# Optimization experiments

Measured on AMD Instinct MI355X. Metric: run time of the kernel, lower is better.

## Reference

```python
import jax, jax.numpy as jnp
import numpy as np

EPS = 1e-5

def _instance_norm(t):
    # torch .var(dim=2) default is unbiased (ddof=1) over flattened HW
    b, c, h, w = t.shape
    flat = t.reshape(b, c, h * w)
    mean = flat.mean(axis=2)
    var = flat.var(axis=2, ddof=1) + EPS
    return (t - mean[:, :, None, None]) / jnp.sqrt(var)[:, :, None, None]

def _conv1x1(t, w, b):
    # w: [Cout, Cin], b: [Cout]; t: [B, Cin, H, W]
    return jnp.einsum('oc,bchw->bohw', w, t) + b[None, :, None, None]


def setup_inputs() -> dict:
    key = jax.random.key(0)
    ks = jax.random.split(key, 11)
    B, C, H, W = 4, 512, 64, 64
    scale = 1.0 / np.sqrt(C)
    inp = {
        'c': jax.random.normal(ks[0], (B, C, H, W), jnp.float32),
        's': jax.random.normal(ks[1], (B, C, H, W), jnp.float32),
        'x': jax.random.normal(ks[2], (B, C, H, W), jnp.float32),
        'c_w': jax.random.normal(ks[3], (C, C), jnp.float32) * scale,
        'c_b': jax.random.normal(ks[4], (C,), jnp.float32) * 0.01,
        's_w': jax.random.normal(ks[5], (C, C), jnp.float32) * scale,
        's_b': jax.random.normal(ks[6], (C,), jnp.float32) * 0.01,
        'i_w': jax.random.normal(ks[7], (C, C), jnp.float32) * scale,
        'i_b': jax.random.normal(ks[8], (C,), jnp.float32) * 0.01,
        'o_w': jax.random.normal(ks[9], (C, C), jnp.float32) * scale,
        'o_b': jax.random.normal(ks[10], (C,), jnp.float32) * 0.01,
    }
    return inp


def reference(c, s, x, c_w, c_b, s_w, s_b, i_w, i_b, o_w, o_b):
    B, C, H, W = c.shape
    N = H * W
    cf = _conv1x1(_instance_norm(c), c_w, c_b).reshape(B, C, N)
    sf = _conv1x1(_instance_norm(s), s_w, s_b).reshape(B, C, N)
    xf = _conv1x1(s, i_w, i_b).reshape(B, C, N)
    # mask[b, n, m] = sum_c cf[b, c, n] * sf[b, c, m]; softmax over m
    mask = jax.nn.softmax(jnp.einsum('bcn,bcm->bnm', cf, sf), axis=-1)
    # of = xf @ mask^T : of[b, c, n] = sum_m xf[b, c, m] * mask[b, n, m]
    of = jnp.einsum('bcm,bnm->bcn', xf, mask).reshape(B, C, H, W)
    of = _conv1x1(of, o_w, o_b)
    return x + of
```

## Files before the change

kernel.cpp:

```cpp
#include <hip/hip_runtime.h>

typedef unsigned short u16;
typedef _Float16 f16x8 __attribute__((ext_vector_type(8)));
typedef float f32x4 __attribute__((ext_vector_type(4)));
typedef u16 u16x4 __attribute__((ext_vector_type(4)));
typedef u16 u16x8v __attribute__((ext_vector_type(8)));

__device__ __forceinline__ u16 f2h(float f) {
    _Float16 h = (_Float16)f;
    return __builtin_bit_cast(u16, h);
}
__device__ __forceinline__ float h2f(u16 u) {
    return (float)__builtin_bit_cast(_Float16, u);
}

__global__ void __launch_bounds__(256) stats_kernel(
    const float* __restrict__ c, const float* __restrict__ s,
    float* __restrict__ mC, float* __restrict__ rC,
    float* __restrict__ mS, float* __restrict__ rS)
{
    const float* src = (blockIdx.y ? s : c) + (size_t)blockIdx.x * 4096;
    int t = threadIdx.x, lane = t & 63, wv = t >> 6;
    const float4* p = (const float4*)src;
    float sum = 0.f, sq = 0.f;
#pragma unroll
    for (int i = 0; i < 4; ++i) {
        float4 v = p[t + 256 * i];
        sum += v.x + v.y + v.z + v.w;
        sq  += v.x * v.x + v.y * v.y + v.z * v.z + v.w * v.w;
    }
#pragma unroll
    for (int m = 1; m < 64; m <<= 1) {
        sum += __shfl_xor(sum, m);
        sq  += __shfl_xor(sq, m);
    }
    __shared__ float sa[4], sb[4];
    if (!lane) { sa[wv] = sum; sb[wv] = sq; }
    __syncthreads();
    if (t == 0) {
        float S = sa[0] + sa[1] + sa[2] + sa[3];
        float Q = sb[0] + sb[1] + sb[2] + sb[3];
        float mean = S * (1.0f / 4096.0f);
        float var = (Q - 4096.0f * mean * mean) * (1.0f / 4095.0f);
        float rstd = rsqrtf(var + 1e-5f);
        if (blockIdx.y) { mS[blockIdx.x] = mean; rS[blockIdx.x] = rstd; }
        else            { mC[blockIdx.x] = mean; rC[blockIdx.x] = rstd; }
    }
}

__global__ void __launch_bounds__(256) packall(
    const float* __restrict__ c, const float* __restrict__ s,
    const float* __restrict__ mC, const float* __restrict__ rC,
    const float* __restrict__ mS, const float* __restrict__ rS,
    u16* __restrict__ cnT, u16* __restrict__ snT, u16* __restrict__ sRT)
{
    __shared__ float tile[32][33];
    int z = blockIdx.z;
    bool isS = z >= 4;
    int b = isS ? z - 4 : z;
    const float* src  = isS ? s : c;
    const float* mean = isS ? mS : mC;
    const float* rstd = isS ? rS : rC;
    u16* dh = isS ? snT : cnT;
    int n0 = blockIdx.x * 32, c0 = blockIdx.y * 32;
    int tx = threadIdx.x, ty = threadIdx.y;
    const float* sbp = src + ((size_t)b * 512 + c0) * 4096 + n0;
#pragma unroll
    for (int it = 0; it < 4; ++it) {
        int cc = ty + it * 8;
        tile[cc][tx] = sbp[(size_t)cc * 4096 + tx];
    }
    __syncthreads();
    int ch = c0 + tx;
    float mn = mean[b * 512 + ch];
    float rs = rstd[b * 512 + ch];
    size_t obase = ((size_t)b * 4096 + n0) * 512 + c0;
#pragma unroll
    for (int it = 0; it < 4; ++it) {
        int r = ty + it * 8;
        float v = tile[tx][r];
        size_t o = obase + (size_t)r * 512 + tx;
        dh[o] = f2h((v - mn) * rs);
        if (isS) sRT[o] = f2h(v);
    }
}

__global__ void __launch_bounds__(256) prep_kernel(
    const float* __restrict__ c_w, const float* __restrict__ s_w,
    const float* __restrict__ i_w, const float* __restrict__ o_w,
    u16* __restrict__ cwT, u16* __restrict__ swT,
    u16* __restrict__ iwT, u16* __restrict__ ow)
{
    int z = blockIdx.z;
    int tx = threadIdx.x, ty = threadIdx.y;
    if (z == 3) {
        size_t base = ((size_t)(blockIdx.y * 16 + blockIdx.x) * 256 +
                       (ty * 32 + tx)) * 4;
        float4 v = *(const float4*)(o_w + base);
        u16x4 o;
        o[0] = f2h(v.x); o[1] = f2h(v.y); o[2] = f2h(v.z); o[3] = f2h(v.w);
        *(u16x4*)(ow + base) = o;
        return;
    }
    const float* w = (z == 0) ? c_w : (z == 1) ? s_w : i_w;
    u16* wT = (z == 0) ? cwT : (z == 1) ? swT : iwT;
    __shared__ float tile[32][33];
    int c0 = blockIdx.x * 32, k0 = blockIdx.y * 32;
#pragma unroll
    for (int it = 0; it < 4; ++it) {
        int kk = ty + it * 8;
        tile[kk][tx] = w[(size_t)(k0 + kk) * 512 + c0 + tx];
    }
    __syncthreads();
#pragma unroll
    for (int it = 0; it < 4; ++it) {
        int r = ty + it * 8;
        wT[(size_t)(c0 + r) * 512 + k0 + tx] = f2h(tile[tx][r]);
    }
}

__global__ void __launch_bounds__(256) bias_prep(
    const float* __restrict__ o_w, const float* __restrict__ i_b,
    const float* __restrict__ o_b, const float* __restrict__ s_w,
    const float* __restrict__ c_b, float* __restrict__ v,
    float* __restrict__ wu)
{
    __shared__ float buf[512];
    int t = threadIdx.x;
    bool isWu = blockIdx.x >= 2;
    const float* vec = isWu ? c_b : i_b;
    buf[t] = vec[t]; buf[t + 256] = vec[t + 256];
    __syncthreads();
    int o = (blockIdx.x & 1) * 256 + t;
    if (!isWu) {
        float acc = o_b[o];
        const float* row = o_w + (size_t)o * 512;
        for (int k = 0; k < 512; ++k) acc += row[k] * buf[k];
        v[o] = acc;
    } else {
        float acc = 0.f;
        for (int k = 0; k < 512; ++k) acc += buf[k] * s_w[(size_t)k * 512 + o];
        wu[o] = acc;
    }
}

__global__ void __launch_bounds__(256) rowdot_kernel(
    const u16* __restrict__ snT, const float* __restrict__ wu,
    float* __restrict__ u)
{
    __shared__ float swu[512];
    int t = threadIdx.x;
    swu[t] = wu[t]; swu[t + 256] = wu[t + 256];
    __syncthreads();
    int lane = t & 63, wv = t >> 6;
    int row = blockIdx.x * 4 + wv;
    u16x8v h = *(const u16x8v*)(snT + (size_t)row * 512 + lane * 8);
    float acc = 0.f;
#pragma unroll
    for (int i = 0; i < 8; ++i) acc += h2f(h[i]) * swu[lane * 8 + i];
#pragma unroll
    for (int m = 1; m < 64; m <<= 1) acc += __shfl_xor(acc, m);
    if (!lane) u[row] = acc;
}

#define EPI_F32       0
#define EPI_PLAIN_F16 2

__device__ __forceinline__ void stageA(
    const u16* __restrict__ g, int ldk, int i0, int k0, char* tile, int wv, int lane)
{
#pragma unroll
    for (int cc = 0; cc < 4; ++cc) {
        int chunk = (wv * 4 + cc) * 64 + lane;
        int row  = chunk >> 3;
        int slot = chunk & 7;
        int gc   = slot ^ (row & 7);
        const u16* gp = g + (size_t)(i0 + row) * ldk + (k0 + gc * 8);
        char* lp = tile + (size_t)(wv * 4 + cc) * 1024;
        __builtin_amdgcn_global_load_lds(
            (const __attribute__((address_space(1))) unsigned int*)gp,
            (__attribute__((address_space(3))) unsigned int*)lp, 16, 0, 0);
    }
}
__device__ __forceinline__ void stageB(
    const u16* __restrict__ g, int ldk, int j0, int k0, char* tile, int wv, int lane)
{
#pragma unroll
    for (int cc = 0; cc < 2; ++cc) {
        int chunk = (wv * 2 + cc) * 64 + lane;
        int row  = chunk >> 3;
        int slot = chunk & 7;
        int gc   = slot ^ (row & 7);
        const u16* gp = g + (size_t)(j0 + row) * ldk + (k0 + gc * 8);
        char* lp = tile + (size_t)(wv * 2 + cc) * 1024;
        __builtin_amdgcn_global_load_lds(
            (const __attribute__((address_space(1))) unsigned int*)gp,
            (__attribute__((address_space(3))) unsigned int*)lp, 16, 0, 0);
    }
}

template<int EPI>
__global__ void __launch_bounds__(512) gemm_bt(
    const u16* __restrict__ A_, const u16* __restrict__ B_,
    int K, int ldk, const float* __restrict__ bias,
    const float* __restrict__ jb, long jbZ,
    float* __restrict__ outF_, u16* __restrict__ outH_,
    int ldo, int zdiv,
    long aBatch, long aChunk, long bBatch, long bChunk, long oZ)
{
    __shared__ char smem[49152];

    int bz = blockIdx.z;
    int batch = bz / zdiv, chunk = bz % zdiv;
    const u16* A  = A_ + (size_t)batch * aBatch + (size_t)chunk * aChunk;
    const u16* Bm = B_ + (size_t)batch * bBatch + (size_t)chunk * bChunk;

    int i0 = blockIdx.y * 256, j0 = blockIdx.x * 128;
    int tid = threadIdx.x, lane = tid & 63, wv = tid >> 6;
    int wr = wv >> 1, wc = wv & 1;
    int r15 = lane & 15, h4 = lane >> 4;

    f32x4 zero = {0.f, 0.f, 0.f, 0.f};
    f32x4 acc[4][4];
#pragma unroll
    for (int m = 0; m < 4; ++m)
#pragma unroll
        for (int n = 0; n < 4; ++n) acc[m][n] = zero;

    for (int k0 = 0; k0 < K; k0 += 64) {
        stageA(A, ldk, i0, k0, smem, wv, lane);
        stageB(Bm, ldk, j0, k0, smem + 32768, wv, lane);
        asm volatile("s_waitcnt vmcnt(0)" ::: "memory");
        __syncthreads();
#pragma unroll
        for (int ks = 0; ks < 2; ++ks) {
            f16x8 a[4], b[4];
#pragma unroll
            for (int m = 0; m < 4; ++m) {
                int row = wr * 64 + m * 16 + r15;
                int off = row * 128 + (((ks * 4 + h4) ^ (row & 7)) << 4);
                a[m] = *(const f16x8*)(smem + off);
            }
#pragma unroll
            for (int n = 0; n < 4; ++n) {
                int col = wc * 64 + n * 16 + r15;
                int off = col * 128 + (((ks * 4 + h4) ^ (col & 7)) << 4);
                b[n] = *(const f16x8*)(smem + 32768 + off);
            }
#pragma unroll
            for (int m = 0; m < 4; ++m)
#pragma unroll
                for (int n = 0; n < 4; ++n)
                    acc[m][n] = __builtin_amdgcn_mfma_f32_16x16x32_f16(a[m], b[n], acc[m][n], 0, 0, 0);
        }
        __syncthreads();
    }

    float* outF = outF_ ? outF_ + (size_t)bz * oZ : nullptr;
    u16* outH = outH_ ? outH_ + (size_t)bz * oZ : nullptr;
    const float* jbp = jb ? jb + (size_t)bz * jbZ : nullptr;

#pragma unroll
    for (int m = 0; m < 4; ++m)
#pragma unroll
        for (int n = 0; n < 4; ++n) {
            int ibase = i0 + wr * 64 + m * 16 + h4 * 4;
            int j = j0 + wc * 64 + n * 16 + r15;
#pragma unroll
            for (int r = 0; r < 4; ++r) {
                int i = ibase + r;
                float v = acc[m][n][r];
                if constexpr (EPI == EPI_PLAIN_F16) {
                    if (bias) v += bias[i];
                    if (jbp) v += jbp[j];
                    outH[(size_t)i * ldo + j] = f2h(v);
                } else {
                    outF[(size_t)i * ldo + j] = v;
                }
            }
        }
}

__device__ __forceinline__ void stageHalf8(
    const u16* __restrict__ g, int ldk, int row0, int k0, char* dst,
    int wv, int lane)
{
#pragma unroll
    for (int cc = 0; cc < 2; ++cc) {
        int chunk = wv * 64 + lane + cc * 512;
        int row  = chunk >> 3;
        int slot = chunk & 7;
        int gc   = slot ^ (row & 7);
        const u16* gp = g + (size_t)(row0 + row) * ldk + (k0 + gc * 8);
        char* lp = dst + (size_t)(wv * 64 + cc * 512) * 16;
        __builtin_amdgcn_global_load_lds(
            (const __attribute__((address_space(1))) unsigned int*)gp,
            (__attribute__((address_space(3))) unsigned int*)lp, 16, 0, 0);
    }
}

__global__ void __launch_bounds__(512) gemm8p(
    const u16* __restrict__ A_, const u16* __restrict__ B_,
    int K, int ldk, const float* __restrict__ bias,
    const float* __restrict__ jb, long jbZ,
    u16* __restrict__ outH_, int ldo, int zdiv,
    long aBatch, long aChunk, long bBatch, long bChunk, long oZ)
{
    extern __shared__ char smem[];

    int bz = blockIdx.z;
    int batch = bz / zdiv, chunk = bz % zdiv;
    const u16* A  = A_ + (size_t)batch * aBatch + (size_t)chunk * aChunk;
    const u16* Bm = B_ + (size_t)batch * bBatch + (size_t)chunk * bChunk;

    int i0 = blockIdx.y * 256, j0 = blockIdx.x * 256;
    int tid = threadIdx.x, lane = tid & 63, wv = tid >> 6;
    int wr = wv >> 2, wc2 = wv & 3;
    int r15 = lane & 15, h4 = lane >> 4;

    f32x4 zero = {0.f, 0.f, 0.f, 0.f};
    f32x4 acc[4][4][2];
#pragma unroll
    for (int q = 0; q < 4; ++q)
#pragma unroll
        for (int m = 0; m < 4; ++m)
#pragma unroll
            for (int n = 0; n < 2; ++n) acc[q][m][n] = zero;

    int nk = K >> 6;
    stageHalf8(A,  ldk, i0,       0, smem,                 wv, lane);
    stageHalf8(Bm, ldk, j0,       0, smem + 32768,         wv, lane);
    stageHalf8(Bm, ldk, j0 + 128, 0, smem + 32768 + 16384, wv, lane);
    stageHalf8(A,  ldk, i0 + 128, 0, smem + 16384,         wv, lane);
    asm volatile("s_waitcnt vmcnt(0)" ::: "memory");
    __builtin_amdgcn_s_barrier();
    asm volatile("" ::: "memory");

    for (int t = 0; t < nk; ++t) {
        char* bufA = smem + (t & 1) * 65536;
        char* bufB = bufA + 32768;
        char* nbuf = smem + ((t + 1) & 1) * 65536;
#pragma unroll
        for (int q = 0; q < 4; ++q) {
            const int mi = (q >= 2) ? 1 : 0;
            const int ni = (q == 1 || q == 2) ? 1 : 0;
            if (t + 1 < nk) {
                int k0 = (t + 1) * 64;
                if (q == 0)      stageHalf8(A,  ldk, i0,       k0, nbuf,                 wv, lane);
                else if (q == 1) stageHalf8(Bm, ldk, j0,       k0, nbuf + 32768,         wv, lane);
                else if (q == 2) stageHalf8(Bm, ldk, j0 + 128, k0, nbuf + 32768 + 16384, wv, lane);
                else             stageHalf8(A,  ldk, i0 + 128, k0, nbuf + 16384,         wv, lane);
                if (q < 3) asm volatile("s_waitcnt vmcnt(6)" ::: "memory");
            } else {
                if (q == 0)      asm volatile("s_waitcnt vmcnt(4)" ::: "memory");
                else if (q == 1) asm volatile("s_waitcnt vmcnt(2)" ::: "memory");
                else if (q == 2) asm volatile("s_waitcnt vmcnt(0)" ::: "memory");
            }
            __builtin_amdgcn_s_barrier();
            asm volatile("" ::: "memory");
            __builtin_amdgcn_sched_barrier(0);
            __builtin_amdgcn_s_setprio(1);
#pragma unroll
            for (int ks = 0; ks < 2; ++ks) {
                f16x8 a[4], b[2];
#pragma unroll
                for (int m = 0; m < 4; ++m) {
                    int row = mi * 128 + wr * 64 + m * 16 + r15;
                    int off = row * 128 + (((ks * 4 + h4) ^ (row & 7)) << 4);
                    a[m] = *(const f16x8*)(bufA + off);
                }
#pragma unroll
                for (int n = 0; n < 2; ++n) {
                    int col = ni * 128 + wc2 * 32 + n * 16 + r15;
                    int off = col * 128 + (((ks * 4 + h4) ^ (col & 7)) << 4);
                    b[n] = *(const f16x8*)(bufB + off);
                }
#pragma unroll
                for (int m = 0; m < 4; ++m)
#pragma unroll
                    for (int n = 0; n < 2; ++n)
                        acc[q][m][n] = __builtin_amdgcn_mfma_f32_16x16x32_f16(a[m], b[n], acc[q][m][n], 0, 0, 0);
            }
            __builtin_amdgcn_s_setprio(0);
            __builtin_amdgcn_sched_barrier(0);
            asm volatile("" ::: "memory");
            __builtin_amdgcn_s_barrier();
        }
    }

    u16* outH = outH_ + (size_t)bz * oZ;
    const float* jbp = jb ? jb + (size_t)bz * jbZ : nullptr;
#pragma unroll
    for (int q = 0; q < 4; ++q) {
        const int mi = (q >= 2) ? 1 : 0;
        const int ni = (q == 1 || q == 2) ? 1 : 0;
#pragma unroll
        for (int m = 0; m < 4; ++m)
#pragma unroll
            for (int n = 0; n < 2; ++n) {
                int ibase = i0 + mi * 128 + wr * 64 + m * 16 + h4 * 4;
                int j = j0 + ni * 128 + wc2 * 32 + n * 16 + r15;
#pragma unroll
                for (int r = 0; r < 4; ++r) {
                    int i = ibase + r;
                    float v = acc[q][m][n][r];
                    if (bias) v += bias[i];
                    if (jbp) v += jbp[j];
                    outH[(size_t)i * ldo + j] = f2h(v);
                }
            }
    }
}

__global__ void __launch_bounds__(256) softmax16(u16* __restrict__ LP)
{
    u16x8v* row = (u16x8v*)(LP + (size_t)blockIdx.x * 4096);
    int t = threadIdx.x, lane = t & 63, wv = t >> 6;
    u16x8v ca = row[t], cb = row[t + 256];
    float va[8], vb[8];
    float mx = -3.4e38f;
#pragma unroll
    for (int i = 0; i < 8; ++i) {
        va[i] = h2f(ca[i]); vb[i] = h2f(cb[i]);
        mx = fmaxf(mx, fmaxf(va[i], vb[i]));
    }
#pragma unroll
    for (int m = 1; m < 64; m <<= 1) mx = fmaxf(mx, __shfl_xor(mx, m));
    __shared__ float sM[4], sS[4];
    if (!lane) sM[wv] = mx;
    __syncthreads();
    mx = fmaxf(fmaxf(sM[0], sM[1]), fmaxf(sM[2], sM[3]));
    float sum = 0.f;
#pragma unroll
    for (int i = 0; i < 8; ++i) {
        va[i] = __expf(va[i] - mx);
        vb[i] = __expf(vb[i] - mx);
        sum += va[i] + vb[i];
    }
#pragma unroll
    for (int m = 1; m < 64; m <<= 1) sum += __shfl_xor(sum, m);
    if (!lane) sS[wv] = sum;
    __syncthreads();
    sum = sS[0] + sS[1] + sS[2] + sS[3];
    float inv = 1.0f / sum;
    u16x8v oa, ob;
#pragma unroll
    for (int i = 0; i < 8; ++i) {
        oa[i] = f2h(va[i] * inv);
        ob[i] = f2h(vb[i] * inv);
    }
    row[t] = oa; row[t + 256] = ob;
}

__global__ void __launch_bounds__(256) reduce4resid(
    const u16* __restrict__ part, const float* __restrict__ xr,
    const float* __restrict__ v, float* __restrict__ out)
{
    const size_t PLANE = 2097152;
    int b = blockIdx.y;
    size_t g8 = ((size_t)blockIdx.x * 256 + threadIdx.x) * 8;
    const u16* p0 = part + (size_t)b * 4 * PLANE + g8;
    float acc[8] = {0.f, 0.f, 0.f, 0.f, 0.f, 0.f, 0.f, 0.f};
#pragma unroll
    for (int k = 0; k < 4; ++k) {
        u16x8v h = *(const u16x8v*)(p0 + (size_t)k * PLANE);
#pragma unroll
        for (int i = 0; i < 8; ++i) acc[i] += h2f(h[i]);
    }
    const float4* xv = (const float4*)(xr + (size_t)b * PLANE + g8);
    float4 x0 = xv[0], x1 = xv[1];
    float vc = v[g8 >> 12];
    float4 o0, o1;
    o0.x = acc[0] + x0.x + vc; o0.y = acc[1] + x0.y + vc;
    o0.z = acc[2] + x0.z + vc; o0.w = acc[3] + x0.w + vc;
    o1.x = acc[4] + x1.x + vc; o1.y = acc[5] + x1.y + vc;
    o1.z = acc[6] + x1.z + vc; o1.w = acc[7] + x1.w + vc;
    float4* op = (float4*)(out + (size_t)b * PLANE + g8);
    op[0] = o0; op[1] = o1;
}

extern "C" void kernel_launch(void* const* d_in, const int* in_sizes, int n_in,
                              void* d_out, int out_size, void* d_ws, size_t ws_size,
                              hipStream_t stream)
{
    const float* c   = (const float*)d_in[0];
    const float* s   = (const float*)d_in[1];
    const float* x   = (const float*)d_in[2];
    const float* c_w = (const float*)d_in[3];
    const float* c_b = (const float*)d_in[4];
    const float* s_w = (const float*)d_in[5];
    const float* s_b = (const float*)d_in[6];
    const float* i_w = (const float*)d_in[7];
    const float* i_b = (const float*)d_in[8];
    const float* o_w = (const float*)d_in[9];
    const float* o_b = (const float*)d_in[10];
    float* out = (float*)d_out;
    char* ws = (char*)d_ws;

    const int B = 4, C = 512, N = 4096;
    const size_t NC = (size_t)N * C;
    const size_t W2 = (size_t)C * C;
    const size_t NN = (size_t)N * N;
    const int SMEM8 = 131072;

    size_t off = 0;
    auto alloc = [&](size_t bytes) { size_t o = off; off += (bytes + 255) & ~(size_t)255; return o; };

    size_t o_meanC = alloc((size_t)B * C * 4);
    size_t o_rstdC = alloc((size_t)B * C * 4);
    size_t o_meanS = alloc((size_t)B * C * 4);
    size_t o_rstdS = alloc((size_t)B * C * 4);
    size_t o_cwT = alloc(W2 * 2);
    size_t o_swT = alloc(W2 * 2);
    size_t o_iwT = alloc(W2 * 2);
    size_t o_ow  = alloc(W2 * 2);
    size_t o_G   = alloc(W2 * 2);
    size_t o_W   = alloc(W2 * 2);
    size_t o_v   = alloc((size_t)C * 4);
    size_t o_wu  = alloc((size_t)C * 4);
    size_t o_u   = alloc((size_t)B * N * 4);
    size_t o_cnT = alloc(B * NC * 2);
    size_t o_snT = alloc(B * NC * 2);
    size_t o_sRT = alloc(B * NC * 2);
    size_t o_sgT = alloc(B * NC * 2);
    size_t o_sW  = alloc(B * NC * 2);
    size_t o_P   = alloc(2 * NN * 2);
    size_t o_pt  = alloc(8 * NC * 2);

    if (ws_size < off) {
        (void)hipMemsetAsync(d_out, 0, (size_t)out_size * 4, stream);
        return;
    }

    float* meanC = (float*)(ws + o_meanC);
    float* rstdC = (float*)(ws + o_rstdC);
    float* meanS = (float*)(ws + o_meanS);
    float* rstdS = (float*)(ws + o_rstdS);
    u16* cwT = (u16*)(ws + o_cwT);
    u16* swT = (u16*)(ws + o_swT);
    u16* iwT = (u16*)(ws + o_iwT);
    u16* ow  = (u16*)(ws + o_ow);
    u16* Gf  = (u16*)(ws + o_G);
    u16* Wf  = (u16*)(ws + o_W);
    float* vb = (float*)(ws + o_v);
    float* wu = (float*)(ws + o_wu);
    float* ub = (float*)(ws + o_u);
    u16* cnT = (u16*)(ws + o_cnT);
    u16* snT = (u16*)(ws + o_snT);
    u16* sRT = (u16*)(ws + o_sRT);
    u16* sgT = (u16*)(ws + o_sgT);
    u16* sW  = (u16*)(ws + o_sW);
    u16* Pb  = (u16*)(ws + o_P);
    u16* partH = (u16*)(ws + o_pt);

    stats_kernel<<<dim3(B * C, 2), 256, 0, stream>>>(c, s, meanC, rstdC, meanS, rstdS);
    packall<<<dim3(N / 32, C / 32, 8), dim3(32, 8), 0, stream>>>(
        c, s, meanC, rstdC, meanS, rstdS, cnT, snT, sRT);
    prep_kernel<<<dim3(16, 16, 4), dim3(32, 8), 0, stream>>>(
        c_w, s_w, i_w, o_w, cwT, swT, iwT, ow);
    bias_prep<<<dim3(4), 256, 0, stream>>>(o_w, i_b, o_b, s_w, c_b, vb, wu);
    gemm_bt<EPI_PLAIN_F16><<<dim3(4, 2, 2), 512, 0, stream>>>(
        cwT, swT, 512, 512, nullptr, nullptr, 0, nullptr, Gf, 512, 1,
        (long)(3 * W2), 0, (long)W2, 0, (long)W2);
    gemm_bt<EPI_PLAIN_F16><<<dim3(4, 16, B), 512, 0, stream>>>(
        snT, Gf, 512, 512, nullptr, nullptr, 0, nullptr, sgT, 512, 1,
        (long)NC, 0, 0, 0, (long)NC);
    gemm_bt<EPI_PLAIN_F16><<<dim3(32, 2, B), 512, 0, stream>>>(
        Wf, sRT, 512, 512, nullptr, nullptr, 0, nullptr, sW, 4096, 1,
        0, 0, (long)NC, 0, (long)NC);
    rowdot_kernel<<<dim3(B * N / 4), 256, 0, stream>>>(snT, wu, ub);
    for (int pb0 = 0; pb0 < B; pb0 += 2) {
        gemm8p<<<dim3(16, 16, 2), 512, SMEM8, stream>>>(
            cnT + (size_t)pb0 * NC, sgT + (size_t)pb0 * NC,
            512, 512, nullptr, ub + (size_t)pb0 * N, (long)N,
            Pb, 4096, 1,
            (long)NC, 0, (long)NC, 0, (long)NN);
        softmax16<<<dim3(2 * N), 256, 0, stream>>>(Pb);
        gemm8p<<<dim3(16, 2, 8), 512, SMEM8, stream>>>(
            sW + (size_t)pb0 * NC, Pb, 1024, 4096, nullptr, nullptr, 0,
            partH, 4096, 4,
            (long)NC, 1024L, (long)NN, 1024L, (long)NC);
        reduce4resid<<<dim3((int)(NC / 2048), 2), 256, 0, stream>>>(
            partH, x + (size_t)pb0 * NC, vb, out + (size_t)pb0 * NC);
    }
}
```

Measured before the change: 395.7 us.

## Reorder gemm8p pipeline to prefetch after compute and switch PV gemm to gemm_bt

Restructures the 8-wave GEMM main loop so each quarter-tile of the next K-slice is prefetched right after the matching compute phase, replacing the issue-then-wait-then-compute ordering and dropping the initial full wait. It also adds a macro for the compute phase. Separately, the attention-times-value GEMM launch moves from gemm8p to the gemm_bt kernel with a 128-wide tile grid (32x2x8) and no dynamic shared memory. The aim is better overlap of loads with MFMA work and a better-suited tile shape for the second GEMM, at the cost of more delicate vmcnt/barrier ordering that could cause races.

```diff
diff --git a/kernel.cpp b/kernel.cpp
--- a/kernel.cpp
+++ b/kernel.cpp
@@ -281,6 +281,33 @@
         }
 }
 
+#define PHASE8(BUFA, BUFB, MI, NI, Q) do {                                   \
+    __builtin_amdgcn_s_setprio(1);                                           \
+    _Pragma("unroll")                                                        \
+    for (int ks = 0; ks < 2; ++ks) {                                         \
+        f16x8 a[4], b[2];                                                    \
+        _Pragma("unroll")                                                    \
+        for (int m = 0; m < 4; ++m) {                                        \
+            int row = (MI) * 128 + wr * 64 + m * 16 + r15;                   \
+            int off = row * 128 + (((ks * 4 + h4) ^ (row & 7)) << 4);        \
+            a[m] = *(const f16x8*)((BUFA) + off);                            \
+        }                                                                    \
+        _Pragma("unroll")                                                    \
+        for (int n = 0; n < 2; ++n) {                                        \
+            int col = (NI) * 128 + wc2 * 32 + n * 16 + r15;                  \
+            int off = col * 128 + (((ks * 4 + h4) ^ (col & 7)) << 4);        \
+            b[n] = *(const f16x8*)((BUFB) + off);                            \
+        }                                                                    \
+        _Pragma("unroll")                                                    \
+        for (int m = 0; m < 4; ++m)                                          \
+            _Pragma("unroll")                                                \
+            for (int n = 0; n < 2; ++n)                                      \
+                acc[Q][m][n] = __builtin_amdgcn_mfma_f32_16x16x32_f16(       \
+                    a[m], b[n], acc[Q][m][n], 0, 0, 0);                      \
+    }                                                                        \
+    __builtin_amdgcn_s_setprio(0);                                           \
+} while (0)
+
 __device__ __forceinline__ void stageHalf8(
     const u16* __restrict__ g, int ldk, int row0, int k0, char* dst,
     int wv, int lane)
@@ -328,64 +355,39 @@
             for (int n = 0; n < 2; ++n) acc[q][m][n] = zero;
 
     int nk = K >> 6;
-    stageHalf8(A,  ldk, i0,       0, smem,                 wv, lane);
-    stageHalf8(Bm, ldk, j0,       0, smem + 32768,         wv, lane);
-    stageHalf8(Bm, ldk, j0 + 128, 0, smem + 32768 + 16384, wv, lane);
-    stageHalf8(A,  ldk, i0 + 128, 0, smem + 16384,         wv, lane);
-    asm volatile("s_waitcnt vmcnt(0)" ::: "memory");
-    __builtin_amdgcn_s_barrier();
-    asm volatile("" ::: "memory");
+    stageHalf8(A,  ldk, i0,       0, smem,         wv, lane);
+    stageHalf8(Bm, ldk, j0,       0, smem + 32768, wv, lane);
+    stageHalf8(Bm, ldk, j0 + 128, 0, smem + 49152, wv, lane);
+    stageHalf8(A,  ldk, i0 + 128, 0, smem + 16384, wv, lane);
 
     for (int t = 0; t < nk; ++t) {
-        char* bufA = smem + (t & 1) * 65536;
-        char* bufB = bufA + 32768;
+        char* buf  = smem + (t & 1) * 65536;
+        char* bufB = buf + 32768;
         char* nbuf = smem + ((t + 1) & 1) * 65536;
-#pragma unroll
-        for (int q = 0; q < 4; ++q) {
-            const int mi = (q >= 2) ? 1 : 0;
-            const int ni = (q == 1 || q == 2) ? 1 : 0;
-            if (t + 1 < nk) {
-                int k0 = (t + 1) * 64;
-                if (q == 0)      stageHalf8(A,  ldk, i0,       k0, nbuf,                 wv, lane);
-                else if (q == 1) stageHalf8(Bm, ldk, j0,       k0, nbuf + 32768,         wv, lane);
-                else if (q == 2) stageHalf8(Bm, ldk, j0 + 128, k0, nbuf + 32768 + 16384, wv, lane);
-                else             stageHalf8(A,  ldk, i0 + 128, k0, nbuf + 16384,         wv, lane);
-                if (q < 3) asm volatile("s_waitcnt vmcnt(6)" ::: "memory");
-            } else {
-                if (q == 0)      asm volatile("s_waitcnt vmcnt(4)" ::: "memory");
-                else if (q == 1) asm volatile("s_waitcnt vmcnt(2)" ::: "memory");
-                else if (q == 2) asm volatile("s_waitcnt vmcnt(0)" ::: "memory");
-            }
-            __builtin_amdgcn_s_barrier();
-            asm volatile("" ::: "memory");
-            __builtin_amdgcn_sched_barrier(0);
-            __builtin_amdgcn_s_setprio(1);
-#pragma unroll
-            for (int ks = 0; ks < 2; ++ks) {
-                f16x8 a[4], b[2];
-#pragma unroll
-                for (int m = 0; m < 4; ++m) {
-                    int row = mi * 128 + wr * 64 + m * 16 + r15;
-                    int off = row * 128 + (((ks * 4 + h4) ^ (row & 7)) << 4);
-                    a[m] = *(const f16x8*)(bufA + off);
-                }
-#pragma unroll
-                for (int n = 0; n < 2; ++n) {
-                    int col = ni * 128 + wc2 * 32 + n * 16 + r15;
-                    int off = col * 128 + (((ks * 4 + h4) ^ (col & 7)) << 4);
-                    b[n] = *(const f16x8*)(bufB + off);
-                }
-#pragma unroll
-                for (int m = 0; m < 4; ++m)
-#pragma unroll
-                    for (int n = 0; n < 2; ++n)
-                        acc[q][m][n] = __builtin_amdgcn_mfma_f32_16x16x32_f16(a[m], b[n], acc[q][m][n], 0, 0, 0);
-            }
-            __builtin_amdgcn_s_setprio(0);
-            __builtin_amdgcn_sched_barrier(0);
-            asm volatile("" ::: "memory");
-            __builtin_amdgcn_s_barrier();
-        }
+        bool pre = (t + 1 < nk);
+        int k1 = (t + 1) * 64;
+        asm volatile("s_waitcnt vmcnt(4)" ::: "memory");
+        __builtin_amdgcn_s_barrier();
+        asm volatile("" ::: "memory");
+        PHASE8(buf, bufB, 0, 0, 0);
+        if (pre) stageHalf8(A, ldk, i0, k1, nbuf, wv, lane);
+        if (pre) { asm volatile("s_waitcnt vmcnt(4)" ::: "memory"); }
+        else     { asm volatile("s_waitcnt vmcnt(2)" ::: "memory"); }
+        __builtin_amdgcn_s_barrier();
+        asm volatile("" ::: "memory");
+        PHASE8(buf, bufB, 0, 1, 1);
+        if (pre) stageHalf8(Bm, ldk, j0, k1, nbuf + 32768, wv, lane);
+        if (pre) { asm volatile("s_waitcnt vmcnt(4)" ::: "memory"); }
+        else     { asm volatile("s_waitcnt vmcnt(0)" ::: "memory"); }
+        __builtin_amdgcn_s_barrier();
+        asm volatile("" ::: "memory");
+        PHASE8(buf, bufB, 1, 1, 2);
+        if (pre) stageHalf8(Bm, ldk, j0 + 128, k1, nbuf + 49152, wv, lane);
+        asm volatile("" ::: "memory");
+        __builtin_amdgcn_s_barrier();
+        asm volatile("" ::: "memory");
+        PHASE8(buf, bufB, 1, 0, 3);
+        if (pre) stageHalf8(A, ldk, i0 + 128, k1, nbuf + 16384, wv, lane);
     }
 
     u16* outH = outH_ + (size_t)bz * oZ;
@@ -576,9 +578,9 @@
             Pb, 4096, 1,
             (long)NC, 0, (long)NC, 0, (long)NN);
         softmax16<<<dim3(2 * N), 256, 0, stream>>>(Pb);
-        gemm8p<<<dim3(16, 2, 8), 512, SMEM8, stream>>>(
+        gemm_bt<EPI_PLAIN_F16><<<dim3(32, 2, 8), 512, 0, stream>>>(
             sW + (size_t)pb0 * NC, Pb, 1024, 4096, nullptr, nullptr, 0,
-            partH, 4096, 4,
+            nullptr, partH, 4096, 4,
             (long)NC, 1024L, (long)NN, 1024L, (long)NC);
         reduce4resid<<<dim3((int)(NC / 2048), 2), 256, 0, stream>>>(
             partH, x + (size_t)pb0 * NC, vb, out + (size_t)pb0 * NC);
```

Measured after the change: 384.9 us. 1.03x faster.
